# Optimization experiments

Measured on AMD Instinct MI355X. Metric: run time of the kernel, lower is better.

Reference implementation:

```python
import jax, jax.numpy as jnp
import numpy as np

D = 256          # d_model
NH = 8           # att_nhead
DA = D // NH     # 32 per-head attention dim
ED = 2 * D       # expand_d_model = 512
HID = 2 * ED     # gated hidden = 1024 (V cat ID_V / U cat ID_U)
H = W = 45
N = H * W
BS = 2
MD = 7           # max_local_dis
WS = 2 * MD + 1  # 15 window size


def silu(x):
    return x * jax.nn.sigmoid(x)


def ln(x, g, b, eps=1e-5):
    m = jnp.mean(x, -1, keepdims=True)
    v = jnp.var(x, -1, keepdims=True)
    return (x - m) * jax.lax.rsqrt(v + eps) * g + b


def seq_to_2d(x):  # [n,bs,c] -> [bs,c,h,w]
    return x.reshape(H, W, x.shape[1], x.shape[2]).transpose(2, 3, 0, 1)


def to_seq(x):  # [bs,c,h,w] -> [n,bs,c]
    return x.transpose(2, 3, 0, 1).reshape(N, x.shape[0], x.shape[1])


def global_gated_attn(Q, K, V, U, Wo, bo):
    # long-term GatedPropagation: Q [n,bs,NH*DA], K [m,bs,NH*DA], V [m,bs,HID], U [n,bs,HID]
    n, bs, _ = Q.shape
    m = K.shape[0]
    q = (Q / np.float32(np.sqrt(DA))).reshape(n, bs, NH, DA)
    k = K.reshape(m, bs, NH, DA)
    v = V.reshape(m, bs, NH, HID // NH)
    attn = jax.nn.softmax(jnp.einsum('nbhd,mbhd->bhnm', q, k), axis=-1)
    out = jnp.einsum('bhnm,mbhe->nbhe', attn, v).reshape(n, bs, HID)
    return (out * U) @ Wo + bo


def local_gated_attn(q2d, k2d, v2d, U, Wrel, brel, Wo, bo):
    # short-term LocalGatedPropagation (dilation=1): 15x15 windowed attention
    bs = q2d.shape[0]
    dv = HID // NH
    q = (q2d / np.float32(np.sqrt(DA))).reshape(bs, NH, DA, H, W)
    k = k2d.reshape(bs, NH, DA, H, W)
    v = v2d.reshape(bs, NH, dv, H, W)
    # relative position bias from scaled q (grouped 1x1 conv) -> [WS*WS, bs, NH, H, W]
    rel = jnp.einsum('bhdyx,hod->obhyx', q, Wrel) + brel.T[:, None, :, None, None]
    kp = jnp.pad(k, ((0, 0), (0, 0), (0, 0), (MD, MD), (MD, MD)))
    vp = jnp.pad(v, ((0, 0), (0, 0), (0, 0), (MD, MD), (MD, MD)))
    valid = jnp.pad(jnp.ones((H, W), q2d.dtype), ((MD, MD), (MD, MD)))
    offs = jnp.arange(WS * WS)

    def score_step(_, o):
        dy, dx = o // WS, o % WS
        ks = jax.lax.dynamic_slice(kp, (0, 0, 0, dy, dx), (bs, NH, DA, H, W))
        mk = jax.lax.dynamic_slice(valid, (dy, dx), (H, W))
        return None, (jnp.einsum('bhdyx,bhdyx->bhyx', q, ks), mk)

    _, (scores, masks) = jax.lax.scan(score_step, None, offs)
    scores = scores + rel                                   # [225,bs,NH,H,W]
    scores = jnp.where(masks[:, None, None] > 0, scores, -1e9)
    attn = jax.nn.softmax(scores, axis=0)                   # softmax over window positions

    def agg_step(acc, oa):
        o, a = oa
        dy, dx = o // WS, o % WS
        vs = jax.lax.dynamic_slice(vp, (0, 0, 0, dy, dx), (bs, NH, dv, H, W))
        return acc + a[:, :, None] * vs, None

    agg, _ = jax.lax.scan(agg_step, jnp.zeros((bs, NH, dv, H, W), q2d.dtype), (offs, attn))
    out = to_seq(agg.reshape(bs, HID, H, W))
    return (out * U) @ Wo + bo


def setup_inputs() -> dict:
    key = jax.random.key(0)
    ks = jax.random.split(key, 16)

    def w(k, *s):
        return jax.random.normal(k, s, jnp.float32) * 0.02

    z = lambda *s: jnp.zeros(s, jnp.float32)
    return {
        'tgt': jax.random.normal(ks[0], (N, BS, D), jnp.float32),
        'curr_id_emb': jax.random.normal(ks[1], (N, BS, D), jnp.float32),
        'ln1_g': jnp.ones((D,), jnp.float32), 'ln1_b': z(D),
        'W_qv': w(ks[2], D, DA * NH + ED), 'b_qv': z(DA * NH + ED),
        'W_u': w(ks[3], D, ED), 'b_u': z(ED),
        'W_idv': w(ks[4], D, ED), 'b_idv': z(ED),
        'lt_Wo': w(ks[5], HID, 2 * D), 'lt_bo': z(2 * D),
        'st_Wrel': w(ks[6], NH, WS * WS, DA), 'st_brel': z(NH, WS * WS),
        'st_Wo': w(ks[7], HID, 2 * D), 'st_bo': z(2 * D),
        'ln2_g': jnp.ones((D,), jnp.float32), 'ln2_b': z(D),
        'idln2_g': jnp.ones((D,), jnp.float32), 'idln2_b': z(D),
        'sa_Wqk': w(ks[8], 2 * D, DA * NH), 'sa_bqk': z(DA * NH),
        'sa_Wv': w(ks[9], 2 * D, HID), 'sa_bv': z(HID),
        'sa_Wu': w(ks[10], 2 * D, HID), 'sa_bu': z(HID),
        'sa_Wo': w(ks[11], HID, 2 * D), 'sa_bo': z(2 * D),
    }


def reference(tgt, curr_id_emb, ln1_g, ln1_b, W_qv, b_qv, W_u, b_u, W_idv, b_idv,
              lt_Wo, lt_bo, st_Wrel, st_brel, st_Wo, st_bo,
              ln2_g, ln2_b, idln2_g, idln2_b,
              sa_Wqk, sa_bqk, sa_Wv, sa_bv, sa_Wu, sa_bu, sa_Wo, sa_bo):
    # GatedPropagationModule.forward, layer_idx=0, curr_id_emb given, eval mode
    _tgt = ln(tgt, ln1_g, ln1_b)
    qv = _tgt @ W_qv + b_qv
    curr_Q = qv[..., :DA * NH]            # Q == K
    curr_V = silu(qv[..., DA * NH:])      # [N,BS,ED]
    curr_U = _tgt @ W_u + b_u
    cat_U = jnp.concatenate([silu(curr_U), jnp.ones_like(curr_U)], -1)   # [N,BS,HID]
    g_ID_V = silu(curr_id_emb @ W_idv + b_idv)                           # fuse_key_value_id
    cat_gV = jnp.concatenate([curr_V, g_ID_V], -1)                       # [N,BS,HID]
    lq = seq_to_2d(curr_Q)
    cat_lV = jnp.concatenate([seq_to_2d(curr_V), seq_to_2d(g_ID_V)], 1)  # [BS,HID,H,W]
    t2 = global_gated_attn(curr_Q, curr_Q, cat_gV, cat_U, lt_Wo, lt_bo)
    t3 = local_gated_attn(lq, lq, cat_lV, cat_U, st_Wrel, st_brel, st_Wo, st_bo)
    new_tgt = tgt + t2[..., :D] + t3[..., :D]
    tgt_id = t2[..., D:] + t3[..., D:]    # tgt_id starts at 0
    x = jnp.concatenate([ln(new_tgt, ln2_g, ln2_b), ln(tgt_id, idln2_g, idln2_b)], -1)
    Qs = x @ sa_Wqk + sa_bqk
    Vs = silu(x @ sa_Wv + sa_bv)
    Us = silu(x @ sa_Wu + sa_bu)
    s2 = global_gated_attn(Qs, Qs, Vs, Us, sa_Wo, sa_bo)
    return new_tgt + s2[..., :D], tgt_id + s2[..., D:]
```

## Files before the change

kernel.cpp:

```cpp
#include <hip/hip_runtime.h>
#include <math.h>

#define NTOK 2025
#define NBS  4050
#define BSZ  2

typedef __attribute__((ext_vector_type(8))) short bf16x8;
typedef __attribute__((ext_vector_type(4))) float f32x4;

__device__ __forceinline__ float silu_f(float v){ return v / (1.f + __expf(-v)); }

__device__ __forceinline__ unsigned short bf16_rne(float f){
  union { float f; unsigned u; } v; v.f = f;
  unsigned u = v.u;
  return (unsigned short)((u + 0x7FFFu + ((u >> 16) & 1u)) >> 16);
}
__device__ __forceinline__ float bf2f(unsigned short u){
  union { unsigned u; float f; } v; v.u = ((unsigned)u)<<16; return v.f;
}
__device__ __forceinline__ bf16x8 zero_bf8(){
  bf16x8 r;
  #pragma unroll
  for (int j=0;j<8;j++) r[j]=0;
  return r;
// ... 183 lines not shown
      }
      if (ROUTE==1){
        if (col < 256)      ((unsigned short*)P0)[(size_t)row*256 + col] = bf16_rne(v*QSC);
        else if (col < 768) ((unsigned short*)P1)[(size_t)row*1024 + col-256] = bf16_rne(silu_f(v));
        else                ((unsigned short*)P2)[(size_t)row*512 + col-768] = bf16_rne(silu_f(v));
      }
      if (ROUTE==2){
        if (col < 256)       ((unsigned short*)P0)[(size_t)row*256 + col] = bf16_rne(v*QSC);
        else if (col < 1280) ((unsigned short*)P1)[(size_t)row*1024 + col-256] = bf16_rne(silu_f(v));
        else                 ((unsigned short*)P2)[(size_t)row*1024 + col-1280] = bf16_rne(silu_f(v));
      }
      if (ROUTE==3){
        if (col < 256) ((float*)P0)[(size_t)row*256 + col] = v + ((const float*)P2)[(size_t)row*256 + col];
        else           ((float*)P1)[(size_t)row*256 + col-256] = v;
      }
      if (ROUTE==4){
        if (col < 256) ((float*)P0)[(size_t)row*256 + col] = v + ((const float*)P1)[(size_t)row*256 + col];
        else           ((float*)P0)[(size_t)NBS*256 + (size_t)row*256 + col-256] = v + ((const float*)P2)[(size_t)row*256 + col-256];
      }
    }
  }
}

__global__ __launch_bounds__(512) void flash_mfma_kernel(
    const unsigned short* __restrict__ Qp, const unsigned short* __restrict__ Vp,
    const unsigned short* __restrict__ Ug, unsigned short* __restrict__ Out,
    int gateW, int ldo)
{
  __shared__ __align__(16) unsigned short Ks[2*64*40];
  __shared__ __align__(16) unsigned Vt2[2*128*36];
  __shared__ __align__(16) unsigned short Pb[8*16*68];

  const int t  = threadIdx.x;
  const int w  = t >> 6;
  const int half = w >> 2;
  const int wl = w & 3;
  const int th = t & 255;
  const int l  = t & 63;
  const int lr = l & 15;
  const int lg = l >> 4;

  const int bid = blockIdx.x + 32*(blockIdx.y + 8*blockIdx.z);
  const int xcd = bid & 7, rrr = bid >> 3;
  const int grp = (rrr >> 5)*8 + xcd;
  const int h = grp >> 1, b = grp & 1;
  const int r0 = (rrr & 31) * 64;

  unsigned short* KsH = &Ks[half*64*40];
  unsigned*       VtH = &Vt2[half*128*36];

  bf16x8 qf = zero_bf8();
  {
    int n = r0 + wl*16 + lr;
    if (n < NTOK) qf = *reinterpret_cast<const bf16x8*>(&Qp[(size_t)(n*2+b)*256 + h*32 + lg*8]);
  }

  f32x4 acc[8];
  #pragma unroll
  for (int i=0;i<8;i++) acc[i] = (f32x4){0.f,0.f,0.f,0.f};
  float lrun = 0.f;

  const f32x4 zero4 = (f32x4){0.f,0.f,0.f,0.f};

  const int key = th & 63, kdh = th >> 6;
  const int kp  = th & 31, vdh = th >> 5;
  const uint4 z4 = make_uint4(0,0,0,0);
  const int ktBase = half*16;

  bf16x8 kReg = zero_bf8();
  uint4 vA0=z4, vA1=z4, vC0=z4, vC1=z4;
  {
    int k0p = ktBase*64;
    int n = k0p + key;
    if (n < NTOK) kReg = *reinterpret_cast<const bf16x8*>(&Qp[(size_t)(n*2+b)*256 + h*32 + kdh*8]);
    int n0i = k0p + kp*2, n1i = n0i + 1;
    const uint4* v0 = reinterpret_cast<const uint4*>(Vp + (size_t)(n0i*2+b)*1024 + h*128 + vdh*16);
    const uint4* v1 = reinterpret_cast<const uint4*>(Vp + (size_t)(n1i*2+b)*1024 + h*128 + vdh*16);
    if (n0i < NTOK){ vA0 = v0[0]; vA1 = v0[1]; }
    if (n1i < NTOK){ vC0 = v1[0]; vC1 = v1[1]; }
  }

  for (int it=0; it<16; it++){
    const int k0 = (ktBase + it)*64;
    __syncthreads();

    *reinterpret_cast<bf16x8*>(&KsH[key*40 + kdh*8]) = kReg;
    {
      unsigned* dst = &VtH[(vdh*16)*36 + kp];
      VPACK2(dst, 36, 0,  vA0.x, vC0.x)
      VPACK2(dst, 36, 2,  vA0.y, vC0.y)
      VPACK2(dst, 36, 4,  vA0.z, vC0.z)
      VPACK2(dst, 36, 6,  vA0.w, vC0.w)
      VPACK2(dst, 36, 8,  vA1.x, vC1.x)
      VPACK2(dst, 36, 10, vA1.y, vC1.y)
      VPACK2(dst, 36, 12, vA1.z, vC1.z)
      VPACK2(dst, 36, 14, vA1.w, vC1.w)
    }
    __syncthreads();

    if (it+1 < 16){
      int k0n = k0 + 64;
      int n = k0n + key;
      kReg = zero_bf8();
      if (n < NTOK) kReg = *reinterpret_cast<const bf16x8*>(&Qp[(size_t)(n*2+b)*256 + h*32 + kdh*8]);
      int n0i = k0n + kp*2, n1i = n0i + 1;
      const uint4* v0 = reinterpret_cast<const uint4*>(Vp + (size_t)(n0i*2+b)*1024 + h*128 + vdh*16);
      const uint4* v1 = reinterpret_cast<const uint4*>(Vp + (size_t)(n1i*2+b)*1024 + h*128 + vdh*16);
      vA0=z4; vA1=z4; vC0=z4; vC1=z4;
      if (n0i < NTOK){ vA0 = v0[0]; vA1 = v0[1]; }
      if (n1i < NTOK){ vC0 = v1[0]; vC1 = v1[1]; }
    }

    f32x4 s[4];
    #pragma unroll
    for (int f=0;f<4;f++){
      bf16x8 kb = *reinterpret_cast<const bf16x8*>(&KsH[(16*f + lr)*40 + lg*8]);
      s[f] = __builtin_amdgcn_mfma_f32_16x16x32_bf16(kb, qf, zero4, 0, 0, 0);
    }

    #pragma unroll
    for (int f=0;f<4;f++)
      #pragma unroll
      for (int r=0;r<4;r++)
        s[f][r] = __expf(s[f][r]);
    if (k0 + 64 > NTOK){
      #pragma unroll
      for (int f=0;f<4;f++)
        #pragma unroll
        for (int r=0;r<4;r++)
          if (k0 + 16*f + 4*lg + r >= NTOK) s[f][r] = 0.f;
    }

    {
      float ps = 0.f;
      #pragma unroll
      for (int f=0;f<4;f++){
        ps += s[f][0]; ps += s[f][1]; ps += s[f][2]; ps += s[f][3];
      }
      ps += __shfl_xor(ps, 16);
      ps += __shfl_xor(ps, 32);
      lrun += ps;
    }

    unsigned short* pb = &Pb[w*16*68];
    #pragma unroll
    for (int f=0;f<4;f++){
      unsigned w0 = (unsigned)bf16_rne(s[f][0]) | ((unsigned)bf16_rne(s[f][1])<<16);
      unsigned w1 = (unsigned)bf16_rne(s[f][2]) | ((unsigned)bf16_rne(s[f][3])<<16);
      *reinterpret_cast<uint2*>(&pb[lr*68 + 16*f + 4*lg]) = make_uint2(w0, w1);
    }
    bf16x8 pa0 = *reinterpret_cast<const bf16x8*>(&pb[lr*68 + 0*32 + lg*8]);
    bf16x8 pa1 = *reinterpret_cast<const bf16x8*>(&pb[lr*68 + 1*32 + lg*8]);

    #pragma unroll
    for (int c=0;c<8;c++){
      bf16x8 vb0 = *reinterpret_cast<const bf16x8*>(&VtH[(c*16+lr)*36 + 0*16 + lg*4]);
      acc[c] = __builtin_amdgcn_mfma_f32_16x16x32_bf16(pa0, vb0, acc[c], 0, 0, 0);
    }
    #pragma unroll
    for (int c=0;c<8;c++){
      bf16x8 vb1 = *reinterpret_cast<const bf16x8*>(&VtH[(c*16+lr)*36 + 1*16 + lg*4]);
      acc[c] = __builtin_amdgcn_mfma_f32_16x16x32_bf16(pa1, vb1, acc[c], 0, 0, 0);
    }
  }

  __syncthreads();
  float* exA = (float*)Vt2;
  float* exM = (float*)Ks;
  const int slot = wl*64 + l;
  if (half == 1){
    exM[slot] = lrun;
    #pragma unroll
    for (int c=0;c<8;c++)
      #pragma unroll
      for (int r=0;r<4;r++) exA[slot*33 + c*4 + r] = acc[c][r];
  }
  __syncthreads();
  if (half == 1) return;

  lrun += exM[slot];
  #pragma unroll
  for (int c=0;c<8;c++)
    #pragma unroll
    for (int r=0;r<4;r++)
      acc[c][r] += exA[slot*33 + c*4 + r];

  float linv[4];
  #pragma unroll
  for (int r=0;r<4;r++) linv[r] = 1.f / __shfl(lrun, lg*4 + r);

  #pragma unroll
  for (int r=0;r<4;r++){
    int n = r0 + wl*16 + lg*4 + r;
    if (n >= NTOK) continue;
    size_t rb = (size_t)(n*2+b);
    const unsigned short* ugr = Ug + rb*gateW;
    unsigned short* orow = Out + rb*ldo + h*128;
    #pragma unroll
    for (int c=0;c<8;c++){
      int dv = c*16 + lr;
      int ch = h*128 + dv;
      float v = acc[c][r]*linv[r];
      if (ch < gateW) v *= bf2f(ugr[ch]);
      orow[dv] = bf16_rne(v);
    }
  }
}

__global__ __launch_bounds__(256) void local_attn_kernel(
    const unsigned short* __restrict__ Qp, const unsigned short* __restrict__ Vp,
    const unsigned short* __restrict__ Ug, const unsigned short* __restrict__ WrelBf,
    const float* __restrict__ brel_g, unsigned short* __restrict__ Out, int ldo)
{
  __shared__ unsigned short scb[45][226];
  __shared__ __align__(16) float ubuf[6720];
  unsigned short* Qs = (unsigned short*)ubuf;
  unsigned short* Wk = Qs + 48*40;
  unsigned short* Abuf = (unsigned short*)ubuf;
  unsigned*       Vt2  = (unsigned*)(ubuf + 1728);

  const int t = threadIdx.x;
  const int w = t>>6, l = t&63;
  const int lr = l&15, lg = l>>4;

  const int bid = blockIdx.x + 45*(blockIdx.y + 8*blockIdx.z);
  const int xcd = bid & 7, rrr = bid >> 3;
  const int grp = (rrr/45)*8 + xcd;
  const int h = grp >> 1, b = grp & 1;
  const int y = rrr % 45;

  const f32x4 zero4 = (f32x4){0.f,0.f,0.f,0.f};
  const unsigned short NEGBF = bf16_rne(-1e9f);

  for (int i=t; i<45*226; i+=256) (&scb[0][0])[i] = NEGBF;

  for (int idx=t; idx<192; idx+=256){
    int row = idx>>2, c = (idx&3)<<3;
    bf16x8 v = zero_bf8();
    if (row < 45) v = *reinterpret_cast<const bf16x8*>(&Qp[(size_t)((y*45+row)*2+b)*256 + h*32 + c]);
    *reinterpret_cast<bf16x8*>(&Qs[row*40 + c]) = v;
  }
  for (int idx=t; idx<960; idx+=256){
    int row = idx>>2, c = (idx&3)<<3;
    bf16x8 v = zero_bf8();
    if (row < 225) v = *reinterpret_cast<const bf16x8*>(&WrelBf[((size_t)h*225 + row)*32 + c]);
    *reinterpret_cast<bf16x8*>(&Wk[row*40 + c]) = v;
  }
  __syncthreads();

  bf16x8 sv[5];
#define S_LOAD(c0v, ncv) { \
  _Pragma("unroll") \
  for (int k=0;k<5;k++){ \
    int idx = t + k*256; \
    sv[k] = zero_bf8(); \
    if (idx < (ncv)*192){ \
      int d = idx/192, r192 = idx - d*192; \
      int row = r192>>2, c = (r192&3)<<3; \
      int yy = y + (c0v) + d - 7; \
      if (yy>=0 && yy<45 && row<45) \
        sv[k] = *reinterpret_cast<const bf16x8*>(&Qp[(size_t)((yy*45+row)*2+b)*256 + h*32 + c]); \
    } } }
#define S_WRITE(c0v, ncv) { \
  _Pragma("unroll") \
  for (int k=0;k<5;k++){ \
    int idx = t + k*256; \
    if (idx < (ncv)*192){ \
      int d = idx/192, r192 = idx - d*192; \
      int row = r192>>2, c = (r192&3)<<3; \
      int yy = y + (c0v) + d - 7; \
      if (yy>=0 && yy<45) \
        *reinterpret_cast<bf16x8*>(&Wk[d*1920 + row*40 + c]) = sv[k]; \
    } } }

  S_LOAD(0, 6)

  for (int fo=w; fo<15; fo+=4){
    bf16x8 wb = *reinterpret_cast<const bf16x8*>(&Wk[(16*fo+lr)*40 + lg*8]);
    int o = 16*fo + lr;
    int dyo = o/15, dxo = o - dyo*15;
    int yyo = y + dyo - 7;
    bool ovalid = (o < 225) && (yyo >= 0) && (yyo < 45);
    float bb = ovalid ? brel_g[h*225+o] : 0.f;
    #pragma unroll
    for (int fa=0; fa<3; fa++){
      bf16x8 qa = *reinterpret_cast<const bf16x8*>(&Qs[(16*fa+lr)*40 + lg*8]);
      f32x4 rr = __builtin_amdgcn_mfma_f32_16x16x32_bf16(qa, wb, zero4, 0, 0, 0);
      if (ovalid){
        #pragma unroll
        for (int r=0;r<4;r++){
          int px = 16*fa + lg*4 + r;
          int xx = px + dxo - 7;
          if (px < 45 && xx >= 0 && xx < 45)
            scb[px][o] = bf16_rne(rr[r] + bb);
        }
      }
    }
  }

  for (int ci=0; ci<3; ci++){
    int c0 = ci*6;
    int nc = (ci<2) ? 6 : 3;
    __syncthreads();
    S_WRITE(c0, nc)
    __syncthreads();
    if (ci==0) S_LOAD(6, 6)
    if (ci==1) S_LOAD(12, 3)
    for (int u=w; u<nc*7; u+=4){
      int d = u/7, pi = u - d*7;
      int dy = c0 + d, yy = y + dy - 7;
      if (yy < 0 || yy >= 45) continue;
      int fa = (0x2110210u >> (4*pi)) & 7;
      int fb = (0x1201210u >> (4*pi)) & 7;
      bf16x8 qa = *reinterpret_cast<const bf16x8*>(&Qs[(16*fa+lr)*40 + lg*8]);
      bf16x8 kb = *reinterpret_cast<const bf16x8*>(&Wk[d*1920 + (16*fb+lr)*40 + lg*8]);
      f32x4 s = __builtin_amdgcn_mfma_f32_16x16x32_bf16(qa, kb, zero4, 0, 0, 0);
      int xx = 16*fb + lr;
      #pragma unroll
      for (int r=0;r<4;r++){
        int px = 16*fa + lg*4 + r;
        int dx = xx - px + 7;
        if (px < 45 && xx < 45 && dx >= 0 && dx < 15){
          int o = dy*15+dx;
          scb[px][o] = bf16_rne(bf2f(scb[px][o]) + s[r]);
        }
      }
    }
  }
  __syncthreads();

  {
    int grp2 = t>>5, lane = t&31;
    for (int px = grp2; px < 45; px += 8){
      float sum = 0.f;
      for (int o=lane; o<225; o+=32){
        float p = __expf(bf2f(scb[px][o]));
        scb[px][o] = bf16_rne(p);
        sum += p;
      }
      #pragma unroll
      for (int off=16; off>0; off>>=1) sum += __shfl_xor(sum, off);
      float inv = 1.f/sum;
      for (int o=lane; o<225; o+=32)
        scb[px][o] = bf16_rne(bf2f(scb[px][o]) * inv);
    }
  }

  f32x4 acc[6];
  #pragma unroll
  for (int i=0;i<6;i++) acc[i]=(f32x4){0.f,0.f,0.f,0.f};

  const int dyLo = (y < 7) ? (7-y) : 0;
  const int dyHi = (y > 37) ? (51-y) : 14;
  const int kp = t&31, vdh = t>>5;
  const uint4 z4 = make_uint4(0,0,0,0);
  uint4 vA0=z4, vA1=z4, vC0=z4, vC1=z4;

#define V_LOAD(dyv) { \
    int yy = y + (dyv) - 7; \
    int xx0 = kp*2 - 7, xx1 = xx0 + 1; \
    const uint4* v0p = reinterpret_cast<const uint4*>(Vp + ((size_t)((yy*45+xx0)*2+b))*1024 + h*128 + vdh*16); \
    const uint4* v1p = reinterpret_cast<const uint4*>(Vp + ((size_t)((yy*45+xx1)*2+b))*1024 + h*128 + vdh*16); \
    vA0=z4; vA1=z4; vC0=z4; vC1=z4; \
    if (xx0 >= 0 && xx0 < 45){ vA0 = v0p[0]; vA1 = v0p[1]; } \
    if (xx1 >= 0 && xx1 < 45){ vC0 = v1p[0]; vC1 = v1p[1]; } }

  V_LOAD(dyLo)

  for (int dy=dyLo; dy<=dyHi; dy++){
    __syncthreads();

    {
      unsigned* A32 = (unsigned*)Abuf;
      for (int i=t; i<48*32; i+=256){
        int px = i>>5, wd = i&31;
        int kk0 = wd*2, kk1 = kk0+1;
        unsigned p0 = 0, p1 = 0;
        if (px < 45){
          int dx0 = kk0 - px, dx1 = kk1 - px;
          if (dx0 >= 0 && dx0 < 15 && kk0 >= 7 && kk0 < 52) p0 = scb[px][dy*15+dx0];
          if (dx1 >= 0 && dx1 < 15 && kk1 >= 7 && kk1 < 52) p1 = scb[px][dy*15+dx1];
        }
        A32[px*36 + wd] = p0 | (p1<<16);
      }
    }
    {
      unsigned* dst = &Vt2[(vdh*16)*36 + kp];
      VPACK2(dst, 36, 0,  vA0.x, vC0.x)
      VPACK2(dst, 36, 2,  vA0.y, vC0.y)
      VPACK2(dst, 36, 4,  vA0.z, vC0.z)
      VPACK2(dst, 36, 6,  vA0.w, vC0.w)
      VPACK2(dst, 36, 8,  vA1.x, vC1.x)
      VPACK2(dst, 36, 10, vA1.y, vC1.y)
      VPACK2(dst, 36, 12, vA1.z, vC1.z)
      VPACK2(dst, 36, 14, vA1.w, vC1.w)
    }
    __syncthreads();

    if (dy < dyHi) V_LOAD(dy+1)

    #pragma unroll
    for (int k6=0; k6<6; k6++){
      int u = w + 4*k6;
      int fa = u>>3, ef = u&7;
      bf16x8 a0 = *reinterpret_cast<const bf16x8*>(&Abuf[(16*fa+lr)*72 + 0*32 + lg*8]);
      bf16x8 b0 = *reinterpret_cast<const bf16x8*>(&Vt2[(ef*16+lr)*36 + 0*16 + lg*4]);
      acc[k6] = __builtin_amdgcn_mfma_f32_16x16x32_bf16(a0, b0, acc[k6], 0,0,0);
      bf16x8 a1 = *reinterpret_cast<const bf16x8*>(&Abuf[(16*fa+lr)*72 + 1*32 + lg*8]);
      bf16x8 b1 = *reinterpret_cast<const bf16x8*>(&Vt2[(ef*16+lr)*36 + 1*16 + lg*4]);
      acc[k6] = __builtin_amdgcn_mfma_f32_16x16x32_bf16(a1, b1, acc[k6], 0,0,0);
    }
  }

  #pragma unroll
  for (int k6=0; k6<6; k6++){
    int u = w + 4*k6;
    int fa = u>>3, ef = u&7;
    #pragma unroll
    for (int r=0;r<4;r++){
      int px = 16*fa + lg*4 + r;
      if (px >= 45) continue;
      int e = ef*16 + lr;
      int n = y*45 + px;
      size_t rb = (size_t)(n*2+b);
      int ch = h*128 + e;
      float v = acc[k6][r];
      if (ch < 512) v *= bf2f(Ug[rb*512 + ch]);
      Out[rb*ldo + ch] = bf16_rne(v);
    }
  }
#undef S_LOAD
#undef S_WRITE
#undef V_LOAD
}

extern "C" void kernel_launch(void* const* d_in, const int* in_sizes, int n_in,
                              void* d_out, int out_size, void* d_ws, size_t ws_size,
                              hipStream_t stream)
{
  const float* tgt    = (const float*)d_in[0];
  const float* id_emb = (const float*)d_in[1];
  const float* ln1_g  = (const float*)d_in[2];
  const float* ln1_b  = (const float*)d_in[3];
  const float* W_qv   = (const float*)d_in[4];
  const float* b_qv   = (const float*)d_in[5];
  const float* W_u    = (const float*)d_in[6];
  const float* b_u    = (const float*)d_in[7];
  const float* W_idv  = (const float*)d_in[8];
  const float* b_idv  = (const float*)d_in[9];
  const float* lt_Wo  = (const float*)d_in[10];
  const float* lt_bo  = (const float*)d_in[11];
  const float* Wrel   = (const float*)d_in[12];
  const float* brel   = (const float*)d_in[13];
  const float* st_Wo  = (const float*)d_in[14];
  const float* st_bo  = (const float*)d_in[15];
  const float* ln2_g  = (const float*)d_in[16];
// ... 24 lines not shown
  unsigned short* WrelBf = (unsigned short*)(ws + 15084032);
  unsigned short* idBf   = (unsigned short*)(ws + 15112832);

  const unsigned* Wcat1   = Wpk;
  const unsigned* Widv_pk = Wpk + 163840;
  const unsigned* WcatT23 = Wpk + 229376;
  const unsigned* Wcat2   = Wpk + 753664;
  const unsigned* WsaWo   = Wpk + 1343488;

  const int M = NBS;
  dim3 blk(256);
  int gx = (M+63)/64;

  convert_kernel<<<10547, blk, 0, stream>>>(W_qv, W_u, W_idv, lt_Wo, st_Wo,
      sa_Wqk, sa_Wv, sa_Wu, sa_Wo, Wrel, id_emb, (unsigned*)Wpk, WrelBf, idBf);

  ln256_kernel<<<M, 256, 0, stream>>>(tgt, ln1_g, ln1_b, tgt_ln);

  gemm_mfma_kernel<1><<<dim3(gx, 20), blk, 0, stream>>>(
      tgt_ln,256, Wcat1,1280, b_qv, b_u, nullptr, Qbuf, Vbuf, Ubuf, M, 256);
  gemm_mfma_kernel<0><<<dim3(gx, 8), blk, 0, stream>>>(
      idBf,256, Widv_pk,512, b_idv, nullptr, nullptr, Vbuf, nullptr, nullptr, M, 256);

  flash_mfma_kernel<<<dim3(32,8,2), dim3(512), 0, stream>>>(Qbuf, Vbuf, Ubuf, Gbig, 512, 2048);
  local_attn_kernel<<<dim3(45,8,2), blk, 0, stream>>>(Qbuf, Vbuf, Ubuf, WrelBf, brel, Gbig+1024, 2048);

  gemm_mfma_kernel<3><<<dim3(gx, 8), blk, 0, stream>>>(
      Gbig,2048, WcatT23,512, lt_bo, st_bo, nullptr, newt, tgtid, (void*)tgt, M, 2048);

  ln_dual_kernel<<<M, 256, 0, stream>>>(newt, tgtid, ln2_g, ln2_b, idln2_g, idln2_b, xbuf);

  gemm_mfma_kernel<2><<<dim3(gx, 36), blk, 0, stream>>>(
      xbuf,512, Wcat2,2304, sa_bqk, sa_bv, sa_bu, Qbuf, Vbuf, Us2, M, 512);

  flash_mfma_kernel<<<dim3(32,8,2), dim3(512), 0, stream>>>(Qbuf, Vbuf, Us2, Gbig, 1024, 2048);

  gemm_mfma_kernel<4><<<dim3(gx, 8), blk, 0, stream>>>(
      Gbig,2048, WsaWo,512, sa_bo, nullptr, nullptr, out, newt, tgtid, M, 1024);
}
```

Before: 304.2 us.

## Fuse global flash and local window attention into one heterogeneous launch

```diff
diff --git a/kernel.cpp b/kernel.cpp
--- a/kernel.cpp
+++ b/kernel.cpp
@@ -229,416 +229,425 @@
   }
 }
 
-__global__ __launch_bounds__(512) void flash_mfma_kernel(
+__global__ __launch_bounds__(512, 6) void attn_fused_kernel(
     const unsigned short* __restrict__ Qp, const unsigned short* __restrict__ Vp,
-    const unsigned short* __restrict__ Ug, unsigned short* __restrict__ Out,
-    int gateW, int ldo)
+    const unsigned short* __restrict__ Ug, unsigned short* __restrict__ OutF,
+    int gateW, int ldo,
+    const unsigned short* __restrict__ WrelBf, const float* __restrict__ brel_g,
+    unsigned short* __restrict__ OutL)
 {
-  __shared__ __align__(16) unsigned short Ks[2*64*40];
-  __shared__ __align__(16) unsigned Vt2[2*128*36];
-  __shared__ __align__(16) unsigned short Pb[8*16*68];
-
-  const int t  = threadIdx.x;
-  const int w  = t >> 6;
-  const int half = w >> 2;
-  const int wl = w & 3;
-  const int th = t & 255;
-  const int l  = t & 63;
-  const int lr = l & 15;
-  const int lg = l >> 4;
-
-  const int bid = blockIdx.x + 32*(blockIdx.y + 8*blockIdx.z);
-  const int xcd = bid & 7, rrr = bid >> 3;
-  const int grp = (rrr >> 5)*8 + xcd;
-  const int h = grp >> 1, b = grp & 1;
-  const int r0 = (rrr & 31) * 64;
-
-  unsigned short* KsH = &Ks[half*64*40];
-  unsigned*       VtH = &Vt2[half*128*36];
-
-  bf16x8 qf = zero_bf8();
-  {
-    int n = r0 + wl*16 + lr;
-    if (n < NTOK) qf = *reinterpret_cast<const bf16x8*>(&Qp[(size_t)(n*2+b)*256 + h*32 + lg*8]);
-  }
-
-  f32x4 acc[8];
-  #pragma unroll
-  for (int i=0;i<8;i++) acc[i] = (f32x4){0.f,0.f,0.f,0.f};
-  float lrun = 0.f;
-
+  __shared__ __align__(16) unsigned char smem[53248];
+  const int t = threadIdx.x;
   const f32x4 zero4 = (f32x4){0.f,0.f,0.f,0.f};
-
-  const int key = th & 63, kdh = th >> 6;
-  const int kp  = th & 31, vdh = th >> 5;
   const uint4 z4 = make_uint4(0,0,0,0);
-  const int ktBase = half*16;
-
-  bf16x8 kReg = zero_bf8();
-  uint4 vA0=z4, vA1=z4, vC0=z4, vC1=z4;
-  {
-    int k0p = ktBase*64;
-    int n = k0p + key;
-    if (n < NTOK) kReg = *reinterpret_cast<const bf16x8*>(&Qp[(size_t)(n*2+b)*256 + h*32 + kdh*8]);
-    int n0i = k0p + kp*2, n1i = n0i + 1;
-    const uint4* v0 = reinterpret_cast<const uint4*>(Vp + (size_t)(n0i*2+b)*1024 + h*128 + vdh*16);
-    const uint4* v1 = reinterpret_cast<const uint4*>(Vp + (size_t)(n1i*2+b)*1024 + h*128 + vdh*16);
-    if (n0i < NTOK){ vA0 = v0[0]; vA1 = v0[1]; }
-    if (n1i < NTOK){ vC0 = v1[0]; vC1 = v1[1]; }
-  }
-
-  for (int it=0; it<16; it++){
-    const int k0 = (ktBase + it)*64;
-    __syncthreads();
-
-    *reinterpret_cast<bf16x8*>(&KsH[key*40 + kdh*8]) = kReg;
+
+  if (blockIdx.x < 512){
+    unsigned short* Ks = (unsigned short*)smem;
+    unsigned*       Vt2 = (unsigned*)(smem + 10240);
+    unsigned short* Pb  = (unsigned short*)(smem + 43008);
+
+    const int w  = t >> 6;
+    const int half = w >> 2;
+    const int wl = w & 3;
+    const int th = t & 255;
+    const int l  = t & 63;
+    const int lr = l & 15;
+    const int lg = l >> 4;
+
+    const int bid = blockIdx.x;
+    const int xcd = bid & 7, rrr = bid >> 3;
+    const int grp = (rrr >> 5)*8 + xcd;
+    const int h = grp >> 1, b = grp & 1;
+    const int r0 = (rrr & 31) * 64;
+
+    unsigned short* KsH = &Ks[half*64*40];
+    unsigned*       VtH = &Vt2[half*128*32];
+
+    bf16x8 qf = zero_bf8();
     {
-      unsigned* dst = &VtH[(vdh*16)*36 + kp];
-      VPACK2(dst, 36, 0,  vA0.x, vC0.x)
-      VPACK2(dst, 36, 2,  vA0.y, vC0.y)
-      VPACK2(dst, 36, 4,  vA0.z, vC0.z)
-      VPACK2(dst, 36, 6,  vA0.w, vC0.w)
-      VPACK2(dst, 36, 8,  vA1.x, vC1.x)
-      VPACK2(dst, 36, 10, vA1.y, vC1.y)
-      VPACK2(dst, 36, 12, vA1.z, vC1.z)
-      VPACK2(dst, 36, 14, vA1.w, vC1.w)
-    }
-    __syncthreads();
-
-    if (it+1 < 16){
-      int k0n = k0 + 64;
-      int n = k0n + key;
-      kReg = zero_bf8();
+      int n = r0 + wl*16 + lr;
+      if (n < NTOK) qf = *reinterpret_cast<const bf16x8*>(&Qp[(size_t)(n*2+b)*256 + h*32 + lg*8]);
+    }
+
+    f32x4 acc[8];
+    #pragma unroll
+    for (int i=0;i<8;i++) acc[i] = (f32x4){0.f,0.f,0.f,0.f};
+    float lrun = 0.f;
+
+    const int key = th & 63, kdh = th >> 6;
+    const int kp  = th & 31, vdh = th >> 5;
+    const int ktBase = half*16;
+
+    bf16x8 kReg = zero_bf8();
+    uint4 vA0=z4, vA1=z4, vC0=z4, vC1=z4;
+    {
+      int k0p = ktBase*64;
+      int n = k0p + key;
       if (n < NTOK) kReg = *reinterpret_cast<const bf16x8*>(&Qp[(size_t)(n*2+b)*256 + h*32 + kdh*8]);
-      int n0i = k0n + kp*2, n1i = n0i + 1;
+      int n0i = k0p + kp*2, n1i = n0i + 1;
       const uint4* v0 = reinterpret_cast<const uint4*>(Vp + (size_t)(n0i*2+b)*1024 + h*128 + vdh*16);
       const uint4* v1 = reinterpret_cast<const uint4*>(Vp + (size_t)(n1i*2+b)*1024 + h*128 + vdh*16);
-      vA0=z4; vA1=z4; vC0=z4; vC1=z4;
       if (n0i < NTOK){ vA0 = v0[0]; vA1 = v0[1]; }
       if (n1i < NTOK){ vC0 = v1[0]; vC1 = v1[1]; }
     }
 
-    f32x4 s[4];
-    #pragma unroll
-    for (int f=0;f<4;f++){
-      bf16x8 kb = *reinterpret_cast<const bf16x8*>(&KsH[(16*f + lr)*40 + lg*8]);
-      s[f] = __builtin_amdgcn_mfma_f32_16x16x32_bf16(kb, qf, zero4, 0, 0, 0);
-    }
-
-    #pragma unroll
-    for (int f=0;f<4;f++)
-      #pragma unroll
-      for (int r=0;r<4;r++)
-        s[f][r] = __expf(s[f][r]);
-    if (k0 + 64 > NTOK){
+    for (int it=0; it<16; it++){
+      const int k0 = (ktBase + it)*64;
+      __syncthreads();
+
+      *reinterpret_cast<bf16x8*>(&KsH[key*40 + kdh*8]) = kReg;
+      {
+        unsigned* Vb = VtH + (vdh*16)*32;
+        #define VP2S(e0, aw, cw) \
+          Vb[(e0)*32   + (kp ^ (((e0)&7)<<2))]       = ((aw)&0xffffu) | ((cw)<<16); \
+          Vb[((e0)+1)*32 + (kp ^ ((((e0)+1)&7)<<2))] = ((aw)>>16)     | ((cw)&0xffff0000u);
+        VP2S(0,  vA0.x, vC0.x)
+        VP2S(2,  vA0.y, vC0.y)
+        VP2S(4,  vA0.z, vC0.z)
+        VP2S(6,  vA0.w, vC0.w)
+        VP2S(8,  vA1.x, vC1.x)
+        VP2S(10, vA1.y, vC1.y)
+        VP2S(12, vA1.z, vC1.z)
+        VP2S(14, vA1.w, vC1.w)
+        #undef VP2S
+      }
+      __syncthreads();
+
+      if (it+1 < 16){
+        int k0n = k0 + 64;
+        int n = k0n + key;
+        kReg = zero_bf8();
+        if (n < NTOK) kReg = *reinterpret_cast<const bf16x8*>(&Qp[(size_t)(n*2+b)*256 + h*32 + kdh*8]);
+        int n0i = k0n + kp*2, n1i = n0i + 1;
+        const uint4* v0 = reinterpret_cast<const uint4*>(Vp + (size_t)(n0i*2+b)*1024 + h*128 + vdh*16);
+        const uint4* v1 = reinterpret_cast<const uint4*>(Vp + (size_t)(n1i*2+b)*1024 + h*128 + vdh*16);
+        vA0=z4; vA1=z4; vC0=z4; vC1=z4;
+        if (n0i < NTOK){ vA0 = v0[0]; vA1 = v0[1]; }
+        if (n1i < NTOK){ vC0 = v1[0]; vC1 = v1[1]; }
+      }
+
+      f32x4 s[4];
+      #pragma unroll
+      for (int f=0;f<4;f++){
+        bf16x8 kb = *reinterpret_cast<const bf16x8*>(&KsH[(16*f + lr)*40 + lg*8]);
+        s[f] = __builtin_amdgcn_mfma_f32_16x16x32_bf16(kb, qf, zero4, 0, 0, 0);
+      }
       #pragma unroll
       for (int f=0;f<4;f++)
         #pragma unroll
         for (int r=0;r<4;r++)
-          if (k0 + 16*f + 4*lg + r >= NTOK) s[f][r] = 0.f;
-    }
-
-    {
-      float ps = 0.f;
-      #pragma unroll
-      for (int f=0;f<4;f++){
-        ps += s[f][0]; ps += s[f][1]; ps += s[f][2]; ps += s[f][3];
-      }
-      ps += __shfl_xor(ps, 16);
-      ps += __shfl_xor(ps, 32);
-      lrun += ps;
-    }
-
-    unsigned short* pb = &Pb[w*16*68];
-    #pragma unroll
-    for (int f=0;f<4;f++){
-      unsigned w0 = (unsigned)bf16_rne(s[f][0]) | ((unsigned)bf16_rne(s[f][1])<<16);
-      unsigned w1 = (unsigned)bf16_rne(s[f][2]) | ((unsigned)bf16_rne(s[f][3])<<16);
-      *reinterpret_cast<uint2*>(&pb[lr*68 + 16*f + 4*lg]) = make_uint2(w0, w1);
-    }
-    bf16x8 pa0 = *reinterpret_cast<const bf16x8*>(&pb[lr*68 + 0*32 + lg*8]);
-    bf16x8 pa1 = *reinterpret_cast<const bf16x8*>(&pb[lr*68 + 1*32 + lg*8]);
-
-    #pragma unroll
-    for (int c=0;c<8;c++){
-      bf16x8 vb0 = *reinterpret_cast<const bf16x8*>(&VtH[(c*16+lr)*36 + 0*16 + lg*4]);
-      acc[c] = __builtin_amdgcn_mfma_f32_16x16x32_bf16(pa0, vb0, acc[c], 0, 0, 0);
-    }
-    #pragma unroll
-    for (int c=0;c<8;c++){
-      bf16x8 vb1 = *reinterpret_cast<const bf16x8*>(&VtH[(c*16+lr)*36 + 1*16 + lg*4]);
-      acc[c] = __builtin_amdgcn_mfma_f32_16x16x32_bf16(pa1, vb1, acc[c], 0, 0, 0);
-    }
-  }
-
-  __syncthreads();
-  float* exA = (float*)Vt2;
-  float* exM = (float*)Ks;
-  const int slot = wl*64 + l;
-  if (half == 1){
-    exM[slot] = lrun;
+          s[f][r] = __expf(s[f][r]);
+      if (k0 + 64 > NTOK){
+        #pragma unroll
+        for (int f=0;f<4;f++)
+          #pragma unroll
+          for (int r=0;r<4;r++)
+            if (k0 + 16*f + 4*lg + r >= NTOK) s[f][r] = 0.f;
+      }
+
+      {
+        float ps = 0.f;
+        #pragma unroll
+        for (int f=0;f<4;f++){
+          ps += s[f][0]; ps += s[f][1]; ps += s[f][2]; ps += s[f][3];
+        }
+        ps += __shfl_xor(ps, 16);
+        ps += __shfl_xor(ps, 32);
+        lrun += ps;
+      }
+
+      unsigned short* pb = &Pb[w*16*40];
+      #pragma unroll
+      for (int f=0;f<2;f++){
+        unsigned w0 = (unsigned)bf16_rne(s[f][0]) | ((unsigned)bf16_rne(s[f][1])<<16);
+        unsigned w1 = (unsigned)bf16_rne(s[f][2]) | ((unsigned)bf16_rne(s[f][3])<<16);
+        *reinterpret_cast<uint2*>(&pb[lr*40 + 16*f + 4*lg]) = make_uint2(w0, w1);
+      }
+      {
+        bf16x8 pa0 = *reinterpret_cast<const bf16x8*>(&pb[lr*40 + lg*8]);
+        #pragma unroll
+        for (int c=0;c<8;c++){
+          bf16x8 vb0 = *reinterpret_cast<const bf16x8*>(&VtH[(c*16+lr)*32 + ((lg*4) ^ ((lr&7)<<2))]);
+          acc[c] = __builtin_amdgcn_mfma_f32_16x16x32_bf16(pa0, vb0, acc[c], 0, 0, 0);
+        }
+      }
+      #pragma unroll
+      for (int f=2;f<4;f++){
+        unsigned w0 = (unsigned)bf16_rne(s[f][0]) | ((unsigned)bf16_rne(s[f][1])<<16);
+        unsigned w1 = (unsigned)bf16_rne(s[f][2]) | ((unsigned)bf16_rne(s[f][3])<<16);
+        *reinterpret_cast<uint2*>(&pb[lr*40 + 16*(f-2) + 4*lg]) = make_uint2(w0, w1);
+      }
+      {
+        bf16x8 pa1 = *reinterpret_cast<const bf16x8*>(&pb[lr*40 + lg*8]);
+        #pragma unroll
+        for (int c=0;c<8;c++){
+          bf16x8 vb1 = *reinterpret_cast<const bf16x8*>(&VtH[(c*16+lr)*32 + ((16 + lg*4) ^ ((lr&7)<<2))]);
+          acc[c] = __builtin_amdgcn_mfma_f32_16x16x32_bf16(pa1, vb1, acc[c], 0, 0, 0);
+        }
+      }
+    }
+
+    __syncthreads();
+    float* exA = (float*)Vt2;
+    float* exM = (float*)Ks;
+    const int slot = wl*64 + l;
+    if (half == 1){
+      exM[slot] = lrun;
+      #pragma unroll
+      for (int c=0;c<8;c++)
+        #pragma unroll
+        for (int r=0;r<4;r++)
+          exA[slot*32 + ((c*4+r) ^ (slot&31))] = acc[c][r];
+    }
+    __syncthreads();
+    if (half == 1) return;
+
+    lrun += exM[slot];
     #pragma unroll
     for (int c=0;c<8;c++)
       #pragma unroll
-      for (int r=0;r<4;r++) exA[slot*33 + c*4 + r] = acc[c][r];
-  }
-  __syncthreads();
-  if (half == 1) return;
-
-  lrun += exM[slot];
-  #pragma unroll
-  for (int c=0;c<8;c++)
-    #pragma unroll
-    for (int r=0;r<4;r++)
-      acc[c][r] += exA[slot*33 + c*4 + r];
-
-  float linv[4];
-  #pragma unroll
-  for (int r=0;r<4;r++) linv[r] = 1.f / __shfl(lrun, lg*4 + r);
-
-  #pragma unroll
-  for (int r=0;r<4;r++){
-    int n = r0 + wl*16 + lg*4 + r;
-    if (n >= NTOK) continue;
-    size_t rb = (size_t)(n*2+b);
-    const unsigned short* ugr = Ug + rb*gateW;
-    unsigned short* orow = Out + rb*ldo + h*128;
-    #pragma unroll
-    for (int c=0;c<8;c++){
-      int dv = c*16 + lr;
-      int ch = h*128 + dv;
-      float v = acc[c][r]*linv[r];
-      if (ch < gateW) v *= bf2f(ugr[ch]);
-      orow[dv] = bf16_rne(v);
-    }
-  }
-}
-
-__global__ __launch_bounds__(256) void local_attn_kernel(
-    const unsigned short* __restrict__ Qp, const unsigned short* __restrict__ Vp,
-    const unsigned short* __restrict__ Ug, const unsigned short* __restrict__ WrelBf,
-    const float* __restrict__ brel_g, unsigned short* __restrict__ Out, int ldo)
-{
-  __shared__ unsigned short scb[45][226];
-  __shared__ __align__(16) float ubuf[6720];
-  unsigned short* Qs = (unsigned short*)ubuf;
-  unsigned short* Wk = Qs + 48*40;
-  unsigned short* Abuf = (unsigned short*)ubuf;
-  unsigned*       Vt2  = (unsigned*)(ubuf + 1728);
-
-  const int t = threadIdx.x;
-  const int w = t>>6, l = t&63;
-  const int lr = l&15, lg = l>>4;
-
-  const int bid = blockIdx.x + 45*(blockIdx.y + 8*blockIdx.z);
-  const int xcd = bid & 7, rrr = bid >> 3;
-  const int grp = (rrr/45)*8 + xcd;
-  const int h = grp >> 1, b = grp & 1;
-  const int y = rrr % 45;
-
-  const f32x4 zero4 = (f32x4){0.f,0.f,0.f,0.f};
-  const unsigned short NEGBF = bf16_rne(-1e9f);
-
-  for (int i=t; i<45*226; i+=256) (&scb[0][0])[i] = NEGBF;
-
-  for (int idx=t; idx<192; idx+=256){
-    int row = idx>>2, c = (idx&3)<<3;
-    bf16x8 v = zero_bf8();
-    if (row < 45) v = *reinterpret_cast<const bf16x8*>(&Qp[(size_t)((y*45+row)*2+b)*256 + h*32 + c]);
-    *reinterpret_cast<bf16x8*>(&Qs[row*40 + c]) = v;
-  }
-  for (int idx=t; idx<960; idx+=256){
-    int row = idx>>2, c = (idx&3)<<3;
-    bf16x8 v = zero_bf8();
-    if (row < 225) v = *reinterpret_cast<const bf16x8*>(&WrelBf[((size_t)h*225 + row)*32 + c]);
-    *reinterpret_cast<bf16x8*>(&Wk[row*40 + c]) = v;
-  }
-  __syncthreads();
-
-  bf16x8 sv[5];
+      for (int r=0;r<4;r++)
+        acc[c][r] += exA[slot*32 + ((c*4+r) ^ (slot&31))];
+
+    float linv[4];
+    #pragma unroll
+    for (int r=0;r<4;r++) linv[r] = 1.f / __shfl(lrun, lg*4 + r);
+
+    #pragma unroll
+    for (int r=0;r<4;r++){
+      int n = r0 + wl*16 + lg*4 + r;
+      if (n >= NTOK) continue;
+      size_t rb = (size_t)(n*2+b);
+      const unsigned short* ugr = Ug + rb*gateW;
+      unsigned short* orow = OutF + rb*ldo + h*128;
+      #pragma unroll
+      for (int c=0;c<8;c++){
+        int dv = c*16 + lr;
+        int ch = h*128 + dv;
+        float v = acc[c][r]*linv[r];
+        if (ch < gateW) v *= bf2f(ugr[ch]);
+        orow[dv] = bf16_rne(v);
+      }
+    }
+    return;
+  }
+
+  {
+    unsigned short* scb = (unsigned short*)smem;
+    float* ubuf = (float*)(smem + 20352);
+    unsigned short* Qs = (unsigned short*)ubuf;
+    unsigned short* Wk = Qs + 48*40;
+    unsigned short* Abuf = (unsigned short*)ubuf;
+    unsigned*       Vt2L = (unsigned*)(ubuf + 1728);
+
+    const int w = t>>6, l = t&63;
+    const int lr = l&15, lg = l>>4;
+
+    const int lbid = blockIdx.x - 512;
+    const int xcd = lbid & 7, rrr = lbid >> 3;
+    const int grp = (rrr/45)*8 + xcd;
+    const int h = grp >> 1, b = grp & 1;
+    const int y = rrr % 45;
+
+    const unsigned short NEGBF = bf16_rne(-1e9f);
+
+    for (int i=t; i<45*226; i+=512) scb[i] = NEGBF;
+
+    for (int idx=t; idx<192; idx+=512){
+      int row = idx>>2, c = (idx&3)<<3;
+      bf16x8 v = zero_bf8();
+      if (row < 45) v = *reinterpret_cast<const bf16x8*>(&Qp[(size_t)((y*45+row)*2+b)*256 + h*32 + c]);
+      *reinterpret_cast<bf16x8*>(&Qs[row*40 + c]) = v;
+    }
+    for (int idx=t; idx<960; idx+=512){
+      int row = idx>>2, c = (idx&3)<<3;
+      bf16x8 v = zero_bf8();
+      if (row < 225) v = *reinterpret_cast<const bf16x8*>(&WrelBf[((size_t)h*225 + row)*32 + c]);
+      *reinterpret_cast<bf16x8*>(&Wk[row*40 + c]) = v;
+    }
+    __syncthreads();
+
+    bf16x8 sv[3];
 #define S_LOAD(c0v, ncv) { \
-  _Pragma("unroll") \
-  for (int k=0;k<5;k++){ \
-    int idx = t + k*256; \
-    sv[k] = zero_bf8(); \
-    if (idx < (ncv)*192){ \
-      int d = idx/192, r192 = idx - d*192; \
-      int row = r192>>2, c = (r192&3)<<3; \
-      int yy = y + (c0v) + d - 7; \
-      if (yy>=0 && yy<45 && row<45) \
-        sv[k] = *reinterpret_cast<const bf16x8*>(&Qp[(size_t)((yy*45+row)*2+b)*256 + h*32 + c]); \
-    } } }
+    _Pragma("unroll") \
+    for (int k=0;k<3;k++){ \
+      int idx = t + k*512; \
+      sv[k] = zero_bf8(); \
+      if (idx < (ncv)*192){ \
+        int d = idx/192, r192 = idx - d*192; \
+        int row = r192>>2, c = (r192&3)<<3; \
+        int yy = y + (c0v) + d - 7; \
+        if (yy>=0 && yy<45 && row<45) \
+          sv[k] = *reinterpret_cast<const bf16x8*>(&Qp[(size_t)((yy*45+row)*2+b)*256 + h*32 + c]); \
+      } } }
 #define S_WRITE(c0v, ncv) { \
-  _Pragma("unroll") \
-  for (int k=0;k<5;k++){ \
-    int idx = t + k*256; \
-    if (idx < (ncv)*192){ \
-      int d = idx/192, r192 = idx - d*192; \
-      int row = r192>>2, c = (r192&3)<<3; \
-      int yy = y + (c0v) + d - 7; \
-      if (yy>=0 && yy<45) \
-        *reinterpret_cast<bf16x8*>(&Wk[d*1920 + row*40 + c]) = sv[k]; \
-    } } }
-
-  S_LOAD(0, 6)
-
-  for (int fo=w; fo<15; fo+=4){
-    bf16x8 wb = *reinterpret_cast<const bf16x8*>(&Wk[(16*fo+lr)*40 + lg*8]);
-    int o = 16*fo + lr;
-    int dyo = o/15, dxo = o - dyo*15;
-    int yyo = y + dyo - 7;
-    bool ovalid = (o < 225) && (yyo >= 0) && (yyo < 45);
-    float bb = ovalid ? brel_g[h*225+o] : 0.f;
-    #pragma unroll
-    for (int fa=0; fa<3; fa++){
-      bf16x8 qa = *reinterpret_cast<const bf16x8*>(&Qs[(16*fa+lr)*40 + lg*8]);
-      f32x4 rr = __builtin_amdgcn_mfma_f32_16x16x32_bf16(qa, wb, zero4, 0, 0, 0);
-      if (ovalid){
+    _Pragma("unroll") \
+    for (int k=0;k<3;k++){ \
+      int idx = t + k*512; \
+      if (idx < (ncv)*192){ \
+        int d = idx/192, r192 = idx - d*192; \
+        int row = r192>>2, c = (r192&3)<<3; \
+        int yy = y + (c0v) + d - 7; \
+        if (yy>=0 && yy<45) \
+          *reinterpret_cast<bf16x8*>(&Wk[d*1920 + row*40 + c]) = sv[k]; \
+      } } }
+
+    S_LOAD(0, 6)
+
+    for (int fo=w; fo<15; fo+=8){
+      bf16x8 wb = *reinterpret_cast<const bf16x8*>(&Wk[(16*fo+lr)*40 + lg*8]);
+      int o = 16*fo + lr;
+      int dyo = o/15, dxo = o - dyo*15;
+      int yyo = y + dyo - 7;
+      bool ovalid = (o < 225) && (yyo >= 0) && (yyo < 45);
+      float bb = ovalid ? brel_g[h*225+o] : 0.f;
+      #pragma unroll
+      for (int fa=0; fa<3; fa++){
+        bf16x8 qa = *reinterpret_cast<const bf16x8*>(&Qs[(16*fa+lr)*40 + lg*8]);
+        f32x4 rr = __builtin_amdgcn_mfma_f32_16x16x32_bf16(qa, wb, zero4, 0, 0, 0);
+        if (ovalid){
+          #pragma unroll
+          for (int r=0;r<4;r++){
+            int px = 16*fa + lg*4 + r;
+            int xx = px + dxo - 7;
+            if (px < 45 && xx >= 0 && xx < 45)
+              scb[px*226 + o] = bf16_rne(rr[r] + bb);
+          }
+        }
+      }
+    }
+
+    for (int ci=0; ci<3; ci++){
+      int c0 = ci*6;
+      int nc = (ci<2) ? 6 : 3;
+      __syncthreads();
+      S_WRITE(c0, nc)
+      __syncthreads();
+      if (ci==0) S_LOAD(6, 6)
+      if (ci==1) S_LOAD(12, 3)
+      for (int u=w; u<nc*7; u+=8){
+        int d = u/7, pi = u - d*7;
+        int dy = c0 + d, yy = y + dy - 7;
+        if (yy < 0 || yy >= 45) continue;
+        int fa = (0x2110210u >> (4*pi)) & 7;
+        int fb = (0x1201210u >> (4*pi)) & 7;
+        bf16x8 qa = *reinterpret_cast<const bf16x8*>(&Qs[(16*fa+lr)*40 + lg*8]);
+        bf16x8 kb = *reinterpret_cast<const bf16x8*>(&Wk[d*1920 + (16*fb+lr)*40 + lg*8]);
+        f32x4 s = __builtin_amdgcn_mfma_f32_16x16x32_bf16(qa, kb, zero4, 0, 0, 0);
+        int xx = 16*fb + lr;
         #pragma unroll
         for (int r=0;r<4;r++){
           int px = 16*fa + lg*4 + r;
-          int xx = px + dxo - 7;
-          if (px < 45 && xx >= 0 && xx < 45)
-            scb[px][o] = bf16_rne(rr[r] + bb);
+          int dx = xx - px + 7;
+          if (px < 45 && xx < 45 && dx >= 0 && dx < 15){
+            int o = dy*15+dx;
+            scb[px*226 + o] = bf16_rne(bf2f(scb[px*226 + o]) + s[r]);
+          }
         }
       }
     }
-  }
-
-  for (int ci=0; ci<3; ci++){
-    int c0 = ci*6;
-    int nc = (ci<2) ? 6 : 3;
     __syncthreads();
-    S_WRITE(c0, nc)
-    __syncthreads();
-    if (ci==0) S_LOAD(6, 6)
-    if (ci==1) S_LOAD(12, 3)
-    for (int u=w; u<nc*7; u+=4){
-      int d = u/7, pi = u - d*7;
-      int dy = c0 + d, yy = y + dy - 7;
-      if (yy < 0 || yy >= 45) continue;
-      int fa = (0x2110210u >> (4*pi)) & 7;
-      int fb = (0x1201210u >> (4*pi)) & 7;
-      bf16x8 qa = *reinterpret_cast<const bf16x8*>(&Qs[(16*fa+lr)*40 + lg*8]);
-      bf16x8 kb = *reinterpret_cast<const bf16x8*>(&Wk[d*1920 + (16*fb+lr)*40 + lg*8]);
-      f32x4 s = __builtin_amdgcn_mfma_f32_16x16x32_bf16(qa, kb, zero4, 0, 0, 0);
-      int xx = 16*fb + lr;
+
+    {
+      int grp2 = t>>5, lane = t&31;
+      for (int px = grp2; px < 45; px += 16){
+        float sum = 0.f;
+        for (int o=lane; o<225; o+=32){
+          float p = __expf(bf2f(scb[px*226 + o]));
+          scb[px*226 + o] = bf16_rne(p);
+          sum += p;
+        }
+        #pragma unroll
+        for (int off=16; off>0; off>>=1) sum += __shfl_xor(sum, off);
+        float inv = 1.f/sum;
+        for (int o=lane; o<225; o+=32)
+          scb[px*226 + o] = bf16_rne(bf2f(scb[px*226 + o]) * inv);
+      }
+    }
+
+    f32x4 acc[3];
+    #pragma unroll
+    for (int i=0;i<3;i++) acc[i]=(f32x4){0.f,0.f,0.f,0.f};
+
+    const int dyLo = (y < 7) ? (7-y) : 0;
+    const int dyHi = (y > 37) ? (51-y) : 14;
+    const int kp = t&31, vg = (t>>5)&7, vs = t>>8;
+    const int rb0 = vg*16 + vs*8;
+    uint4 vA0=z4, vC0=z4;
+
+#define V_LOAD(dyv) { \
+      int yy = y + (dyv) - 7; \
+      int xx0 = kp*2 - 7, xx1 = xx0 + 1; \
+      const uint4* v0p = reinterpret_cast<const uint4*>(Vp + ((size_t)((yy*45+xx0)*2+b))*1024 + h*128 + rb0); \
+      const uint4* v1p = reinterpret_cast<const uint4*>(Vp + ((size_t)((yy*45+xx1)*2+b))*1024 + h*128 + rb0); \
+      vA0=z4; vC0=z4; \
+      if (xx0 >= 0 && xx0 < 45) vA0 = v0p[0]; \
+      if (xx1 >= 0 && xx1 < 45) vC0 = v1p[0]; }
+
+    V_LOAD(dyLo)
+
+    for (int dy=dyLo; dy<=dyHi; dy++){
+      __syncthreads();
+
+      {
+        unsigned* A32 = (unsigned*)Abuf;
+        for (int i=t; i<48*32; i+=512){
+          int px = i>>5, wd = i&31;
+          int kk0 = wd*2, kk1 = kk0+1;
+          unsigned p0 = 0, p1 = 0;
+          if (px < 45){
+            int dx0 = kk0 - px, dx1 = kk1 - px;
+            if (dx0 >= 0 && dx0 < 15 && kk0 >= 7 && kk0 < 52) p0 = scb[px*226 + dy*15+dx0];
+            if (dx1 >= 0 && dx1 < 15 && kk1 >= 7 && kk1 < 52) p1 = scb[px*226 + dy*15+dx1];
+          }
+          A32[px*36 + wd] = p0 | (p1<<16);
+        }
+      }
+      {
+        unsigned* dst = &Vt2L[rb0*36 + kp];
+        VPACK2(dst, 36, 0, vA0.x, vC0.x)
+        VPACK2(dst, 36, 2, vA0.y, vC0.y)
+        VPACK2(dst, 36, 4, vA0.z, vC0.z)
+        VPACK2(dst, 36, 6, vA0.w, vC0.w)
+      }
+      __syncthreads();
+
+      if (dy < dyHi) V_LOAD(dy+1)
+
+      #pragma unroll
+      for (int k3=0; k3<3; k3++){
+        int u = w + 8*k3;
+        int fa = u>>3, ef = u&7;
+        bf16x8 a0 = *reinterpret_cast<const bf16x8*>(&Abuf[(16*fa+lr)*72 + 0*32 + lg*8]);
+        bf16x8 b0 = *reinterpret_cast<const bf16x8*>(&Vt2L[(ef*16+lr)*36 + 0*16 + lg*4]);
+        acc[k3] = __builtin_amdgcn_mfma_f32_16x16x32_bf16(a0, b0, acc[k3], 0,0,0);
+        bf16x8 a1 = *reinterpret_cast<const bf16x8*>(&Abuf[(16*fa+lr)*72 + 1*32 + lg*8]);
+        bf16x8 b1 = *reinterpret_cast<const bf16x8*>(&Vt2L[(ef*16+lr)*36 + 1*16 + lg*4]);
+        acc[k3] = __builtin_amdgcn_mfma_f32_16x16x32_bf16(a1, b1, acc[k3], 0,0,0);
+      }
+    }
+
+    #pragma unroll
+    for (int k3=0; k3<3; k3++){
+      int u = w + 8*k3;
+      int fa = u>>3, ef = u&7;
       #pragma unroll
       for (int r=0;r<4;r++){
         int px = 16*fa + lg*4 + r;
-        int dx = xx - px + 7;
-        if (px < 45 && xx < 45 && dx >= 0 && dx < 15){
-          int o = dy*15+dx;
-          scb[px][o] = bf16_rne(bf2f(scb[px][o]) + s[r]);
-        }
-      }
-    }
-  }
-  __syncthreads();
-
-  {
-    int grp2 = t>>5, lane = t&31;
-    for (int px = grp2; px < 45; px += 8){
-      float sum = 0.f;
-      for (int o=lane; o<225; o+=32){
-        float p = __expf(bf2f(scb[px][o]));
-        scb[px][o] = bf16_rne(p);
-        sum += p;
-      }
-      #pragma unroll
-      for (int off=16; off>0; off>>=1) sum += __shfl_xor(sum, off);
-      float inv = 1.f/sum;
-      for (int o=lane; o<225; o+=32)
-        scb[px][o] = bf16_rne(bf2f(scb[px][o]) * inv);
-    }
-  }
-
-  f32x4 acc[6];
-  #pragma unroll
-  for (int i=0;i<6;i++) acc[i]=(f32x4){0.f,0.f,0.f,0.f};
-
-  const int dyLo = (y < 7) ? (7-y) : 0;
-  const int dyHi = (y > 37) ? (51-y) : 14;
-  const int kp = t&31, vdh = t>>5;
-  const uint4 z4 = make_uint4(0,0,0,0);
-  uint4 vA0=z4, vA1=z4, vC0=z4, vC1=z4;
-
-#define V_LOAD(dyv) { \
-    int yy = y + (dyv) - 7; \
-    int xx0 = kp*2 - 7, xx1 = xx0 + 1; \
-    const uint4* v0p = reinterpret_cast<const uint4*>(Vp + ((size_t)((yy*45+xx0)*2+b))*1024 + h*128 + vdh*16); \
-    const uint4* v1p = reinterpret_cast<const uint4*>(Vp + ((size_t)((yy*45+xx1)*2+b))*1024 + h*128 + vdh*16); \
-    vA0=z4; vA1=z4; vC0=z4; vC1=z4; \
-    if (xx0 >= 0 && xx0 < 45){ vA0 = v0p[0]; vA1 = v0p[1]; } \
-    if (xx1 >= 0 && xx1 < 45){ vC0 = v1p[0]; vC1 = v1p[1]; } }
-
-  V_LOAD(dyLo)
-
-  for (int dy=dyLo; dy<=dyHi; dy++){
-    __syncthreads();
-
-    {
-      unsigned* A32 = (unsigned*)Abuf;
-      for (int i=t; i<48*32; i+=256){
-        int px = i>>5, wd = i&31;
-        int kk0 = wd*2, kk1 = kk0+1;
-        unsigned p0 = 0, p1 = 0;
-        if (px < 45){
-          int dx0 = kk0 - px, dx1 = kk1 - px;
-          if (dx0 >= 0 && dx0 < 15 && kk0 >= 7 && kk0 < 52) p0 = scb[px][dy*15+dx0];
-          if (dx1 >= 0 && dx1 < 15 && kk1 >= 7 && kk1 < 52) p1 = scb[px][dy*15+dx1];
-        }
-        A32[px*36 + wd] = p0 | (p1<<16);
-      }
-    }
-    {
-      unsigned* dst = &Vt2[(vdh*16)*36 + kp];
-      VPACK2(dst, 36, 0,  vA0.x, vC0.x)
-      VPACK2(dst, 36, 2,  vA0.y, vC0.y)
-      VPACK2(dst, 36, 4,  vA0.z, vC0.z)
-      VPACK2(dst, 36, 6,  vA0.w, vC0.w)
-      VPACK2(dst, 36, 8,  vA1.x, vC1.x)
-      VPACK2(dst, 36, 10, vA1.y, vC1.y)
-      VPACK2(dst, 36, 12, vA1.z, vC1.z)
-      VPACK2(dst, 36, 14, vA1.w, vC1.w)
-    }
-    __syncthreads();
-
-    if (dy < dyHi) V_LOAD(dy+1)
-
-    #pragma unroll
-    for (int k6=0; k6<6; k6++){
-      int u = w + 4*k6;
-      int fa = u>>3, ef = u&7;
-      bf16x8 a0 = *reinterpret_cast<const bf16x8*>(&Abuf[(16*fa+lr)*72 + 0*32 + lg*8]);
-      bf16x8 b0 = *reinterpret_cast<const bf16x8*>(&Vt2[(ef*16+lr)*36 + 0*16 + lg*4]);
-      acc[k6] = __builtin_amdgcn_mfma_f32_16x16x32_bf16(a0, b0, acc[k6], 0,0,0);
-      bf16x8 a1 = *reinterpret_cast<const bf16x8*>(&Abuf[(16*fa+lr)*72 + 1*32 + lg*8]);
-      bf16x8 b1 = *reinterpret_cast<const bf16x8*>(&Vt2[(ef*16+lr)*36 + 1*16 + lg*4]);
-      acc[k6] = __builtin_amdgcn_mfma_f32_16x16x32_bf16(a1, b1, acc[k6], 0,0,0);
-    }
-  }
-
-  #pragma unroll
-  for (int k6=0; k6<6; k6++){
-    int u = w + 4*k6;
-    int fa = u>>3, ef = u&7;
-    #pragma unroll
-    for (int r=0;r<4;r++){
-      int px = 16*fa + lg*4 + r;
-      if (px >= 45) continue;
-      int e = ef*16 + lr;
-      int n = y*45 + px;
-      size_t rb = (size_t)(n*2+b);
-      int ch = h*128 + e;
-      float v = acc[k6][r];
-      if (ch < 512) v *= bf2f(Ug[rb*512 + ch]);
-      Out[rb*ldo + ch] = bf16_rne(v);
-    }
-  }
+        if (px >= 45) continue;
+        int e = ef*16 + lr;
+        int n = y*45 + px;
+        size_t rb = (size_t)(n*2+b);
+        int ch = h*128 + e;
+        float v = acc[k3][r];
+        if (ch < 512) v *= bf2f(Ug[rb*512 + ch]);
+        OutL[rb*ldo + ch] = bf16_rne(v);
+      }
+    }
 #undef S_LOAD
 #undef S_WRITE
 #undef V_LOAD
+  }
 }
 
 extern "C" void kernel_launch(void* const* d_in, const int* in_sizes, int n_in,
@@ -709,8 +718,8 @@
   gemm_mfma_kernel<0><<<dim3(gx, 8), blk, 0, stream>>>(
       idBf,256, Widv_pk,512, b_idv, nullptr, nullptr, Vbuf, nullptr, nullptr, M, 256);
 
-  flash_mfma_kernel<<<dim3(32,8,2), dim3(512), 0, stream>>>(Qbuf, Vbuf, Ubuf, Gbig, 512, 2048);
-  local_attn_kernel<<<dim3(45,8,2), blk, 0, stream>>>(Qbuf, Vbuf, Ubuf, WrelBf, brel, Gbig+1024, 2048);
+  attn_fused_kernel<<<dim3(1232), dim3(512), 0, stream>>>(
+      Qbuf, Vbuf, Ubuf, Gbig, 512, 2048, WrelBf, brel, Gbig+1024);
 
   gemm_mfma_kernel<3><<<dim3(gx, 8), blk, 0, stream>>>(
       Gbig,2048, WcatT23,512, lt_bo, st_bo, nullptr, newt, tgtid, (void*)tgt, M, 2048);
@@ -720,7 +729,8 @@
   gemm_mfma_kernel<2><<<dim3(gx, 36), blk, 0, stream>>>(
       xbuf,512, Wcat2,2304, sa_bqk, sa_bv, sa_bu, Qbuf, Vbuf, Us2, M, 512);
 
-  flash_mfma_kernel<<<dim3(32,8,2), dim3(512), 0, stream>>>(Qbuf, Vbuf, Us2, Gbig, 1024, 2048);
+  attn_fused_kernel<<<dim3(512), dim3(512), 0, stream>>>(
+      Qbuf, Vbuf, Us2, Gbig, 1024, 2048, WrelBf, brel, Gbig+1024);
 
   gemm_mfma_kernel<4><<<dim3(gx, 8), blk, 0, stream>>>(
       Gbig,2048, WsaWo,512, sa_bo, nullptr, nullptr, out, newt, tgtid, M, 1024);
```

Measured after the change: 460.7 us. +51.5%, slower.
